# Performance work log

Hardware: AMD Instinct MI355X
Metric: run time of the kernel (lower is better)

The kernel has to match this reference:

```python
import jax, jax.numpy as jnp
import numpy as np

GROUPS = 8
EPS = 1e-5


def group_norm(x, gamma, beta):
    # x: (b, c, h, w); normalize per sample over each group of c//GROUPS channels and all spatial dims
    b, c, h, w = x.shape
    xg = x.reshape(b, GROUPS, c // GROUPS, h, w)
    mean = jnp.mean(xg, axis=(2, 3, 4), keepdims=True)
    var = jnp.var(xg, axis=(2, 3, 4), keepdims=True)
    xn = ((xg - mean) * jax.lax.rsqrt(var + EPS)).reshape(b, c, h, w)
    return xn * gamma[None, :, None, None] + beta[None, :, None, None]


def setup_inputs() -> dict:
    key = jax.random.key(0)
    k1, k2, k3 = jax.random.split(key, 3)
    b, c, h, w = 32, 256, 32, 32
    x = jax.random.normal(k1, (b, c, h, w), dtype=jnp.float32)
    qkv_w = jax.random.normal(k2, (3 * c, c), dtype=jnp.float32) * 0.02
    qkv_b = jnp.zeros((3 * c,), dtype=jnp.float32)
    out_w = jax.random.normal(k3, (c, c), dtype=jnp.float32) * 0.02
    out_b = jnp.zeros((c,), dtype=jnp.float32)
    gn_gamma = jnp.ones((c,), dtype=jnp.float32)
    gn_beta = jnp.zeros((c,), dtype=jnp.float32)
    return {"x": x, "gn_gamma": gn_gamma, "gn_beta": gn_beta,
            "qkv_w": qkv_w, "qkv_b": qkv_b, "out_w": out_w, "out_b": out_b}


def reference(x, gn_gamma, gn_beta, qkv_w, qkv_b, out_w, out_b):
    b, c, h, w = x.shape
    xn = group_norm(x, gn_gamma, gn_beta)
    # 1x1 conv == per-pixel linear: (b,c,h,w) x (3c,c) -> (b,3c,h,w)
    qkv = jnp.einsum('bchw,dc->bdhw', xn, qkv_w) + qkv_b[None, :, None, None]
    q, k, v = jnp.split(qkv, 3, axis=1)
    # (b, c, h, w) -> (b, hw, c)
    def tok(t):
        return t.transpose(0, 2, 3, 1).reshape(b, h * w, c)
    q, k, v = tok(q), tok(k), tok(v)
    scale = 1.0 / jnp.sqrt(jnp.asarray(c, dtype=x.dtype))
    scores = jnp.einsum('bnc,bmc->bnm', q, k) * scale  # (b, hw, hw)
    attn = jax.nn.softmax(scores, axis=-1)
    out = jnp.einsum('bnm,bmc->bnc', attn, v)  # (b, hw, c)
    out = out.reshape(b, h, w, c).transpose(0, 3, 1, 2)  # (b, c, h, w)
    out = jnp.einsum('bchw,dc->bdhw', out, out_w) + out_b[None, :, None, None]
    return out + x
```

## Files before the change

kernel.cpp:

```cpp
#include <hip/hip_runtime.h>
#include <hip/hip_bf16.h>
#include <stdint.h>


typedef __bf16 bf16_t;
typedef __bf16 bf16x4 __attribute__((ext_vector_type(4)));
typedef __bf16 bf16x8 __attribute__((ext_vector_type(8)));
typedef float f32x16 __attribute__((ext_vector_type(16)));
typedef _Float16 f16x4 __attribute__((ext_vector_type(4)));

#define MFMA32(a, b, c) __builtin_amdgcn_mfma_f32_32x32x16_bf16((a), (b), (c), 0, 0, 0)
#define GLL16(g, l)                                                                      \
    __builtin_amdgcn_global_load_lds((const __attribute__((address_space(1))) void*)(g), \
                                     (__attribute__((address_space(3))) void*)(l), 16, 0, 0)
#define WAITV0 asm volatile("s_waitcnt vmcnt(0)" ::: "memory")
#define SBAR   __builtin_amdgcn_s_barrier()

#define QSCALE 0.0901684400555f

__global__ void cast_w(const float* __restrict__ s1, bf16_t* __restrict__ d1, int n1,
                       const float* __restrict__ s2, bf16_t* __restrict__ d2, int n2) {
    int i = blockIdx.x * blockDim.x + threadIdx.x;
    int stride = gridDim.x * blockDim.x;
    for (int k = i; k < n1; k += stride) d1[k] = (bf16_t)s1[k];
    for (int k = i; k < n2; k += stride) d2[k] = (bf16_t)s2[k];
}

__global__ __launch_bounds__(512) void gn_kernel(const float* __restrict__ x,
                                                 const float* __restrict__ gamma,
                                                 const float* __restrict__ beta,
                                                 bf16_t* __restrict__ xn) {
    extern __shared__ char gsm[];
    float* red = (float*)(gsm + 65536);
    int bg = blockIdx.x, b = bg >> 3, g = bg & 7;
    const float* base = x + (size_t)(b * 256 + g * 32) * 1024;
    int tid = threadIdx.x;
    int half = tid >> 8, col = tid & 255;

    float s = 0.f, ss = 0.f;
    #pragma unroll 4
    for (int c2 = 0; c2 < 16; c2++) {
        int c = c2 * 2 + half;
        float4 v = *(const float4*)(base + c * 1024 + col * 4);
        s += v.x + v.y + v.z + v.w;
        ss += v.x * v.x + v.y * v.y + v.z * v.z + v.w * v.w;
        f16x4 h = {(_Float16)v.x, (_Float16)v.y, (_Float16)v.z, (_Float16)v.w};
        *(f16x4*)(gsm + c * 2048 + ((col * 8) ^ ((c & 7) << 4))) = h;
    }
    for (int off = 32; off; off >>= 1) { s += __shfl_down(s, off); ss += __shfl_down(ss, off); }
    if ((tid & 63) == 0) { red[tid >> 6] = s; red[8 + (tid >> 6)] = ss; }
    __syncthreads();
    float S = 0.f, SS = 0.f;
    #pragma unroll
    for (int k = 0; k < 8; k++) { S += red[k]; SS += red[8 + k]; }
    float mean = S * (1.0f / 32768.0f);
    float var = SS * (1.0f / 32768.0f) - mean * mean;
    float rstd = rsqrtf(var + 1e-5f);

    int c = tid & 31;
    float gam = gamma[g * 32 + c] * rstd;
    float bet = beta[g * 32 + c] - mean * gam;
    bf16_t* dst = xn + (size_t)(b * 1024) * 256 + g * 32 + c;
    #pragma unroll 4
    for (int it = 0; it < 64; it++) {
        int p = it * 16 + (tid >> 5);
        _Float16 hv = *(_Float16*)(gsm + c * 2048 + ((p * 2) ^ ((c & 7) << 4)));
        dst[(size_t)p * 256] = (bf16_t)((float)hv * gam + bet);
    }
}

__global__ __launch_bounds__(512, 2) void gemm_qkv(const bf16_t* __restrict__ xn,
                                                   const bf16_t* __restrict__ wq,
                                                   const float* __restrict__ qkv_b,
                                                   bf16_t* __restrict__ qb,
                                                   bf16_t* __restrict__ kb,
                                                   bf16_t* __restrict__ vt) {
    extern __shared__ char smem[];
    char* As = smem;
    int tid = threadIdx.x, wv = tid >> 6, lane = tid & 63;
    int l31 = lane & 31, hi = lane >> 5;
    int t0 = blockIdx.x * 128;
    const char* asrc = (const char*)xn + (size_t)t0 * 512;
    const char* wsrc = (const char*)wq;

    {
        int u = lane & 31, rofs = lane >> 5;
        #pragma unroll
        for (int t = 0; t < 8; t++) {
            int r0 = wv * 16 + t * 2;
            int r = r0 + rofs;
            GLL16(asrc + (size_t)r * 512 + ((u ^ (r & 31)) * 16), As + r0 * 512);
        }
    }
    auto stage_B = [&](int nt) {
        char* Bd = smem + 65536 + (nt & 1) * 32768;
        int u = lane & 31, rofs = lane >> 5;
        #pragma unroll
        for (int t = 0; t < 4; t++) {
            int r0 = wv * 8 + t * 2;
            int r = r0 + rofs;
            GLL16(wsrc + (size_t)(nt * 64 + r) * 512 + ((u ^ (r & 31)) * 16), Bd + r0 * 512);
        }
    };
    stage_B(0);
    WAITV0; SBAR;

    int wm = wv >> 1, wd = wv & 1;
    int bb = t0 >> 10, pos0 = t0 & 1023;

    for (int nt = 0; nt < 12; nt++) {
        if (nt < 11) stage_B(nt + 1);
        const char* Bs = smem + 65536 + (nt & 1) * 32768;
        f32x16 acc = {};
        if (nt < 8) {
            __builtin_amdgcn_s_setprio(1);
            #pragma unroll
            for (int ks = 0; ks < 16; ks++) {
                int col = ks * 32 + hi * 16;
                bf16x8 a = *(const bf16x8*)(As + (wm * 32 + l31) * 512 + (col ^ (l31 << 4)));
                bf16x8 bfr = *(const bf16x8*)(Bs + (wd * 32 + l31) * 512 + (col ^ (l31 << 4)));
                acc = MFMA32(a, bfr, acc);
            }
            __builtin_amdgcn_s_setprio(0);
            int d = nt * 64 + wd * 32 + l31;
            bool isq = nt < 4;
            float bias = qkv_b[d];
            bf16_t* dst = isq ? qb : kb;
            int dd = isq ? d : d - 256;
            float sc = isq ? QSCALE : 1.0f;
            #pragma unroll
            for (int r = 0; r < 16; r++) {
                int tok = t0 + wm * 32 + (r & 3) + 8 * (r >> 2) + 4 * hi;
                dst[(size_t)tok * 256 + dd] = (bf16_t)((acc[r] + bias) * sc);
            }
        } else {
            __builtin_amdgcn_s_setprio(1);
            #pragma unroll
            for (int ks = 0; ks < 16; ks++) {
                int col = ks * 32 + hi * 16;
                bf16x8 a = *(const bf16x8*)(As + (wm * 32 + l31) * 512 + (col ^ (l31 << 4)));
                bf16x8 bfr = *(const bf16x8*)(Bs + (wd * 32 + l31) * 512 + (col ^ (l31 << 4)));
                acc = MFMA32(bfr, a, acc);
            }
            __builtin_amdgcn_s_setprio(0);
            int dbase = (nt - 8) * 64 + wd * 32;
            int pos = pos0 + wm * 32 + l31;
            #pragma unroll
            for (int r = 0; r < 16; r++) {
                int d = dbase + (r & 3) + 8 * (r >> 2) + 4 * hi;
                vt[(size_t)bb * 262144 + (size_t)d * 1024 + pos] =
                    (bf16_t)(acc[r] + qkv_b[512 + d]);
            }
        }
        if (nt < 11) { WAITV0; SBAR; }
    }
}

__global__ __launch_bounds__(256, 1) void attn_kernel(const bf16_t* __restrict__ qb,
                                                      const bf16_t* __restrict__ kb,
                                                      const bf16_t* __restrict__ vt,
                                                      bf16_t* __restrict__ ao) {
    extern __shared__ char smem[];
    int tid = threadIdx.x, i = blockIdx.x;
    int b = (i & 7) + ((i >> 6) << 3);
    int qt = (i >> 3) & 7;
    int wv = tid >> 6, lane = tid & 63, l31 = lane & 31, hi = lane >> 5;

    const char* kbase = (const char*)kb + (size_t)b * 524288;
    const char* vbase = (const char*)vt + (size_t)b * 524288;
    char* Pw = smem + 131072 + wv * 4096;

    int qg = qt * 128 + wv * 32 + l31;
    const char* qsrc = (const char*)qb + (size_t)(b * 1024 + qg) * 512;
    bf16x8 qf[16];
    #pragma unroll
    for (int ks = 0; ks < 16; ks++) qf[ks] = *(const bf16x8*)(qsrc + ks * 32 + hi * 16);

    f32x16 o[8] = {};
    float mrun = -1e30f, lrun = 0.f;

    auto stage = [&](int ch) {
        char* Kd = smem + (ch & 1) * 32768;
        char* Vd = smem + 65536 + (ch & 1) * 32768;
        int j0 = ch * 64;
        #pragma unroll
        for (int t = 0; t < 8; t++) {
            int r0 = wv * 16 + t * 2;
            int r = r0 + (lane >> 5), u = lane & 31;
            GLL16(kbase + (size_t)(j0 + r) * 512 + ((u ^ (r & 31)) * 16), Kd + r0 * 512);
        }
        #pragma unroll
        for (int h = 0; h < 2; h++) {
            #pragma unroll
            for (int p = 0; p < 4; p++) {
                int Ls = (tid << 4) + (p << 12);
                int s = Ls ^ (((Ls >> 9) & 31) << 4);
                GLL16(vbase + (size_t)(s >> 6) * 2048 + j0 * 2 + h * 64 + (s & 63),
                      Vd + h * 16384 + (p << 12) + wv * 1024);
            }
        }
    };

    stage(0);
    __syncthreads();

    for (int ch = 0; ch < 16; ch++) {
        const char* Ks = smem + (ch & 1) * 32768;
        const char* Vs = smem + 65536 + (ch & 1) * 32768;
        if (ch < 15) stage(ch + 1);

        f32x16 sv0 = {}, sv1 = {};
        #pragma unroll
        for (int ks = 0; ks < 16; ks++) {
            int col = ks * 32 + hi * 16;
            bf16x8 k0 = *(const bf16x8*)(Ks + l31 * 512 + (col ^ (l31 << 4)));
            bf16x8 k1 = *(const bf16x8*)(Ks + (32 + l31) * 512 + (col ^ (l31 << 4)));
            sv0 = MFMA32(k0, qf[ks], sv0);
            sv1 = MFMA32(k1, qf[ks], sv1);
        }

        float mc = -1e30f;
        #pragma unroll
        for (int r = 0; r < 16; r++) mc = fmaxf(mc, fmaxf(sv0[r], sv1[r]));
        mc = fmaxf(mc, __shfl_xor(mc, 32));
        float mo = mrun;
        float mn = (mc <= mo + 8.0f) ? mo : mc;
        float rs = 0.f;
        #pragma unroll
        for (int r = 0; r < 16; r++) {
            sv0[r] = exp2f(sv0[r] - mn);
            sv1[r] = exp2f(sv1[r] - mn);
            rs += sv0[r] + sv1[r];
        }
        rs += __shfl_xor(rs, 32);
        float al = exp2f(mo - mn);
        lrun = lrun * al + rs;
        mrun = mn;

        #pragma unroll
        for (int rg = 0; rg < 4; rg++) {
            bf16x4 pa, pb;
            #pragma unroll
            for (int r = 0; r < 4; r++) {
                pa[r] = (bf16_t)sv0[rg * 4 + r];
                pb[r] = (bf16_t)sv1[rg * 4 + r];
            }
            int sw = (l31 & 7) << 4;
            *(bf16x4*)(Pw + l31 * 128 + ((rg * 16 + hi * 8) ^ sw)) = pa;
            *(bf16x4*)(Pw + l31 * 128 + ((64 + rg * 16 + hi * 8) ^ sw)) = pb;
        }
        if (__any(mn != mo)) {
            #pragma unroll
            for (int dt = 0; dt < 8; dt++) o[dt] = o[dt] * al;
        }

        #pragma unroll
        for (int pk = 0; pk < 4; pk++) {
            int pcol = (pk * 32 + hi * 16) ^ ((l31 & 7) << 4);
            bf16x8 pf = *(const bf16x8*)(Pw + l31 * 128 + pcol);
            const char* Vh = Vs + (pk >> 1) * 16384;
            #pragma unroll
            for (int dt = 0; dt < 8; dt++) {
                int d = dt * 32 + l31;
                int a = (d * 64 + (pk & 1) * 32 + hi * 16) ^ (((d >> 3) & 31) << 4);
                bf16x8 vf = *(const bf16x8*)(Vh + a);
                o[dt] = MFMA32(vf, pf, o[dt]);
            }
        }
        __syncthreads();
    }

    float inv = 1.0f / lrun;
    char* aod = (char*)ao + (size_t)(b * 1024 + qg) * 512;
    #pragma unroll
    for (int dt = 0; dt < 8; dt++) {
        #pragma unroll
        for (int rg = 0; rg < 4; rg++) {
            bf16x4 w;
            #pragma unroll
            for (int r = 0; r < 4; r++) w[r] = (bf16_t)(o[dt][rg * 4 + r] * inv);
            *(bf16x4*)(aod + dt * 64 + rg * 16 + hi * 8) = w;
        }
    }
}

__global__ __launch_bounds__(512, 2) void gemm_out(const bf16_t* __restrict__ wo,
                                                   const bf16_t* __restrict__ ao,
                                                   const float* __restrict__ out_b,
                                                   const float* __restrict__ x,
                                                   float* __restrict__ out) {
    extern __shared__ char smem[];
    char* Bs = smem;
    int tid = threadIdx.x, wv = tid >> 6, lane = tid & 63;
    int l31 = lane & 31, hi = lane >> 5;
    int t0 = blockIdx.x * 128;
    const char* bsrc = (const char*)ao + (size_t)t0 * 512;
    const char* wsrc = (const char*)wo;

    {
        int u = lane & 31, rofs = lane >> 5;
        #pragma unroll
        for (int t = 0; t < 8; t++) {
            int r0 = wv * 16 + t * 2;
            int r = r0 + rofs;
            GLL16(bsrc + (size_t)r * 512 + ((u ^ (r & 31)) * 16), Bs + r0 * 512);
        }
    }
    auto stage_W = [&](int ct) {
        char* Wd = smem + 65536 + (ct & 1) * 32768;
        int u = lane & 31, rofs = lane >> 5;
        #pragma unroll
        for (int t = 0; t < 4; t++) {
            int r0 = wv * 8 + t * 2;
            int r = r0 + rofs;
            GLL16(wsrc + (size_t)(ct * 64 + r) * 512 + ((u ^ (r & 31)) * 16), Wd + r0 * 512);
        }
    };
    stage_W(0);
    WAITV0; SBAR;

    int wm = wv >> 1, wc = wv & 1;
    int bb = t0 >> 10, pos0 = t0 & 1023;

    for (int ct = 0; ct < 4; ct++) {
        if (ct < 3) stage_W(ct + 1);
        const char* Ws = smem + 65536 + (ct & 1) * 32768;
        f32x16 acc = {};
        __builtin_amdgcn_s_setprio(1);
        #pragma unroll
        for (int ks = 0; ks < 16; ks++) {
            int col = ks * 32 + hi * 16;
            bf16x8 w = *(const bf16x8*)(Ws + (wc * 32 + l31) * 512 + (col ^ (l31 << 4)));
            bf16x8 bf = *(const bf16x8*)(Bs + (wm * 32 + l31) * 512 + (col ^ (l31 << 4)));
            acc = MFMA32(w, bf, acc);
        }
        __builtin_amdgcn_s_setprio(0);
        int pos = pos0 + wm * 32 + l31;
        #pragma unroll
        for (int r = 0; r < 16; r++) {
            int c = ct * 64 + wc * 32 + (r & 3) + 8 * (r >> 2) + 4 * hi;
            size_t idx = ((size_t)bb * 256 + c) * 1024 + pos;
            out[idx] = acc[r] + out_b[c] + x[idx];
        }
        if (ct < 3) { WAITV0; SBAR; }
    }
}

extern "C" void kernel_launch(void* const* d_in, const int* in_sizes, int n_in,
                              void* d_out, int out_size, void* d_ws, size_t ws_size,
                              hipStream_t stream) {
    (void)in_sizes; (void)n_in; (void)out_size; (void)ws_size;
    const float* x      = (const float*)d_in[0];
    const float* gamma  = (const float*)d_in[1];
    const float* beta   = (const float*)d_in[2];
    const float* qkv_w  = (const float*)d_in[3];
    const float* qkv_b  = (const float*)d_in[4];
    const float* out_w  = (const float*)d_in[5];
    const float* out_b  = (const float*)d_in[6];
    float* out = (float*)d_out;

    char* ws = (char*)d_ws;
    const size_t MB16 = 16777216;
    bf16_t* xn  = (bf16_t*)(ws);
    bf16_t* qb  = (bf16_t*)(ws + 1 * MB16);
    bf16_t* kb  = (bf16_t*)(ws + 2 * MB16);
    bf16_t* vt  = (bf16_t*)(ws + 3 * MB16);
    bf16_t* ao  = (bf16_t*)(ws + 4 * MB16);
    bf16_t* wqb = (bf16_t*)(ws + 5 * MB16);
    bf16_t* wob = (bf16_t*)(ws + 5 * MB16 + 393216);

    cast_w<<<256, 256, 0, stream>>>(qkv_w, wqb, 196608, out_w, wob, 65536);
    gn_kernel<<<256, 512, 65600, stream>>>(x, gamma, beta, xn);
    gemm_qkv<<<256, 512, 131072, stream>>>(xn, wqb, qkv_b, qb, kb, vt);
    attn_kernel<<<256, 256, 147456, stream>>>(qb, kb, vt, ao);
    gemm_out<<<256, 512, 131072, stream>>>(wob, ao, out_b, x, out);
}
```

Before: 125.4 us.

## Rewrite attention with 16x16 MFMA tiles, smaller chunks and two blocks per CU

The attention kernel moves from 32x32x16 MFMA to 16x16x32 MFMA, with 16 query rows per wave, 64 queries per block and 32-key chunks. LDS drops from 147KB to 68KB and launch_bounds allows 2 blocks per CU, with 512 blocks launched instead of 256. The aim is higher occupancy and less per-wave register pressure, so memory latency is better hidden. In exchange each wave does less MFMA work per LDS load, K/V are restaged twice as often, and the K/V LDS swizzles are rewritten.

```diff
diff --git a/kernel.cpp b/kernel.cpp
--- a/kernel.cpp
+++ b/kernel.cpp
@@ -6,10 +6,12 @@
 typedef __bf16 bf16_t;
 typedef __bf16 bf16x4 __attribute__((ext_vector_type(4)));
 typedef __bf16 bf16x8 __attribute__((ext_vector_type(8)));
+typedef float f32x4 __attribute__((ext_vector_type(4)));
 typedef float f32x16 __attribute__((ext_vector_type(16)));
 typedef _Float16 f16x4 __attribute__((ext_vector_type(4)));
 
 #define MFMA32(a, b, c) __builtin_amdgcn_mfma_f32_32x32x16_bf16((a), (b), (c), 0, 0, 0)
+#define MFMA16(a, b, c) __builtin_amdgcn_mfma_f32_16x16x32_bf16((a), (b), (c), 0, 0, 0)
 #define GLL16(g, l)                                                                      \
     __builtin_amdgcn_global_load_lds((const __attribute__((address_space(1))) void*)(g), \
                                      (__attribute__((address_space(3))) void*)(l), 16, 0, 0)
@@ -156,131 +158,122 @@
     }
 }
 
-__global__ __launch_bounds__(256, 1) void attn_kernel(const bf16_t* __restrict__ qb,
+__global__ __launch_bounds__(256, 2) void attn_kernel(const bf16_t* __restrict__ qb,
                                                       const bf16_t* __restrict__ kb,
                                                       const bf16_t* __restrict__ vt,
                                                       bf16_t* __restrict__ ao) {
     extern __shared__ char smem[];
     int tid = threadIdx.x, i = blockIdx.x;
-    int b = (i & 7) + ((i >> 6) << 3);
-    int qt = (i >> 3) & 7;
-    int wv = tid >> 6, lane = tid & 63, l31 = lane & 31, hi = lane >> 5;
+    int b = (i & 7) + ((i >> 7) << 3);
+    int qt = (i >> 3) & 15;
+    int wv = tid >> 6, lane = tid & 63;
+    int q15 = lane & 15, g = lane >> 4;
 
     const char* kbase = (const char*)kb + (size_t)b * 524288;
     const char* vbase = (const char*)vt + (size_t)b * 524288;
-    char* Pw = smem + 131072 + wv * 4096;
-
-    int qg = qt * 128 + wv * 32 + l31;
-    const char* qsrc = (const char*)qb + (size_t)(b * 1024 + qg) * 512;
-    bf16x8 qf[16];
+    char* Pw = smem + 65536 + wv * 1024;
+
+    int qrow = qt * 64 + wv * 16 + q15;
+    const char* qsrc = (const char*)qb + (size_t)(b * 1024 + qrow) * 512;
+    bf16x8 qf[8];
     #pragma unroll
-    for (int ks = 0; ks < 16; ks++) qf[ks] = *(const bf16x8*)(qsrc + ks * 32 + hi * 16);
-
-    f32x16 o[8] = {};
+    for (int f = 0; f < 8; f++) qf[f] = *(const bf16x8*)(qsrc + f * 64 + g * 16);
+
+    f32x4 o16[16] = {};
     float mrun = -1e30f, lrun = 0.f;
 
     auto stage = [&](int ch) {
-        char* Kd = smem + (ch & 1) * 32768;
-        char* Vd = smem + 65536 + (ch & 1) * 32768;
-        int j0 = ch * 64;
-        #pragma unroll
-        for (int t = 0; t < 8; t++) {
-            int r0 = wv * 16 + t * 2;
-            int r = r0 + (lane >> 5), u = lane & 31;
-            GLL16(kbase + (size_t)(j0 + r) * 512 + ((u ^ (r & 31)) * 16), Kd + r0 * 512);
-        }
-        #pragma unroll
-        for (int h = 0; h < 2; h++) {
-            #pragma unroll
-            for (int p = 0; p < 4; p++) {
-                int Ls = (tid << 4) + (p << 12);
-                int s = Ls ^ (((Ls >> 9) & 31) << 4);
-                GLL16(vbase + (size_t)(s >> 6) * 2048 + j0 * 2 + h * 64 + (s & 63),
-                      Vd + h * 16384 + (p << 12) + wv * 1024);
-            }
+        char* Kd = smem + (ch & 1) * 16384;
+        char* Vd = smem + 32768 + (ch & 1) * 16384;
+        int j0 = ch * 32;
+        #pragma unroll
+        for (int p = 0; p < 4; p++) {
+            int Ls = tid * 16 + p * 4096;
+            int r = Ls >> 9, u = (Ls >> 4) & 31;
+            int fk = ((r & 7) << 2) ^ (r >> 3);
+            GLL16(kbase + (size_t)(j0 + r) * 512 + ((u ^ fk) << 4),
+                  Kd + p * 4096 + wv * 1024);
+        }
+        #pragma unroll
+        for (int p = 0; p < 4; p++) {
+            int Ls = tid * 16 + p * 4096;
+            int d = Ls >> 6, u2 = (Ls >> 4) & 3;
+            GLL16(vbase + (size_t)d * 2048 + j0 * 2 + ((u2 ^ ((d >> 3) & 3)) << 4),
+                  Vd + p * 4096 + wv * 1024);
         }
     };
 
     stage(0);
     __syncthreads();
 
-    for (int ch = 0; ch < 16; ch++) {
-        const char* Ks = smem + (ch & 1) * 32768;
-        const char* Vs = smem + 65536 + (ch & 1) * 32768;
-        if (ch < 15) stage(ch + 1);
-
-        f32x16 sv0 = {}, sv1 = {};
-        #pragma unroll
-        for (int ks = 0; ks < 16; ks++) {
-            int col = ks * 32 + hi * 16;
-            bf16x8 k0 = *(const bf16x8*)(Ks + l31 * 512 + (col ^ (l31 << 4)));
-            bf16x8 k1 = *(const bf16x8*)(Ks + (32 + l31) * 512 + (col ^ (l31 << 4)));
-            sv0 = MFMA32(k0, qf[ks], sv0);
-            sv1 = MFMA32(k1, qf[ks], sv1);
-        }
-
-        float mc = -1e30f;
-        #pragma unroll
-        for (int r = 0; r < 16; r++) mc = fmaxf(mc, fmaxf(sv0[r], sv1[r]));
+    int fk0 = ((q15 & 7) << 2) ^ (q15 >> 3);
+    int kr1 = 16 + q15;
+    int fk1 = ((kr1 & 7) << 2) ^ (kr1 >> 3);
+
+    for (int ch = 0; ch < 32; ch++) {
+        const char* Ks = smem + (ch & 1) * 16384;
+        const char* Vs = smem + 32768 + (ch & 1) * 16384;
+        if (ch < 31) stage(ch + 1);
+
+        f32x4 sv0 = {}, sv1 = {};
+        #pragma unroll
+        for (int f = 0; f < 8; f++) {
+            int c = f * 4 + g;
+            bf16x8 k0 = *(const bf16x8*)(Ks + q15 * 512 + ((c ^ fk0) << 4));
+            bf16x8 k1 = *(const bf16x8*)(Ks + kr1 * 512 + ((c ^ fk1) << 4));
+            sv0 = MFMA16(k0, qf[f], sv0);
+            sv1 = MFMA16(k1, qf[f], sv1);
+        }
+
+        float mc = fmaxf(fmaxf(fmaxf(sv0[0], sv0[1]), fmaxf(sv0[2], sv0[3])),
+                         fmaxf(fmaxf(sv1[0], sv1[1]), fmaxf(sv1[2], sv1[3])));
+        mc = fmaxf(mc, __shfl_xor(mc, 16));
         mc = fmaxf(mc, __shfl_xor(mc, 32));
         float mo = mrun;
         float mn = (mc <= mo + 8.0f) ? mo : mc;
         float rs = 0.f;
         #pragma unroll
-        for (int r = 0; r < 16; r++) {
+        for (int r = 0; r < 4; r++) {
             sv0[r] = exp2f(sv0[r] - mn);
             sv1[r] = exp2f(sv1[r] - mn);
             rs += sv0[r] + sv1[r];
         }
+        rs += __shfl_xor(rs, 16);
         rs += __shfl_xor(rs, 32);
         float al = exp2f(mo - mn);
         lrun = lrun * al + rs;
         mrun = mn;
 
-        #pragma unroll
-        for (int rg = 0; rg < 4; rg++) {
-            bf16x4 pa, pb;
-            #pragma unroll
-            for (int r = 0; r < 4; r++) {
-                pa[r] = (bf16_t)sv0[rg * 4 + r];
-                pb[r] = (bf16_t)sv1[rg * 4 + r];
-            }
-            int sw = (l31 & 7) << 4;
-            *(bf16x4*)(Pw + l31 * 128 + ((rg * 16 + hi * 8) ^ sw)) = pa;
-            *(bf16x4*)(Pw + l31 * 128 + ((64 + rg * 16 + hi * 8) ^ sw)) = pb;
-        }
+        bf16x4 pa, pb;
+        #pragma unroll
+        for (int r = 0; r < 4; r++) { pa[r] = (bf16_t)sv0[r]; pb[r] = (bf16_t)sv1[r]; }
+        int blk0 = (g >> 1) ^ (q15 & 3);
+        int blk1 = ((g >> 1) + 2) ^ (q15 & 3);
+        *(bf16x4*)(Pw + q15 * 64 + blk0 * 16 + (g & 1) * 8) = pa;
+        *(bf16x4*)(Pw + q15 * 64 + blk1 * 16 + (g & 1) * 8) = pb;
         if (__any(mn != mo)) {
             #pragma unroll
-            for (int dt = 0; dt < 8; dt++) o[dt] = o[dt] * al;
-        }
-
-        #pragma unroll
-        for (int pk = 0; pk < 4; pk++) {
-            int pcol = (pk * 32 + hi * 16) ^ ((l31 & 7) << 4);
-            bf16x8 pf = *(const bf16x8*)(Pw + l31 * 128 + pcol);
-            const char* Vh = Vs + (pk >> 1) * 16384;
-            #pragma unroll
-            for (int dt = 0; dt < 8; dt++) {
-                int d = dt * 32 + l31;
-                int a = (d * 64 + (pk & 1) * 32 + hi * 16) ^ (((d >> 3) & 31) << 4);
-                bf16x8 vf = *(const bf16x8*)(Vh + a);
-                o[dt] = MFMA32(vf, pf, o[dt]);
-            }
+            for (int dt = 0; dt < 16; dt++) o16[dt] = o16[dt] * al;
+        }
+
+        bf16x8 pf = *(const bf16x8*)(Pw + q15 * 64 + ((g ^ (q15 & 3)) << 4));
+        #pragma unroll
+        for (int dt = 0; dt < 16; dt++) {
+            int d = dt * 16 + q15;
+            bf16x8 vf = *(const bf16x8*)(Vs + d * 64 + ((g ^ ((d >> 3) & 3)) << 4));
+            o16[dt] = MFMA16(vf, pf, o16[dt]);
         }
         __syncthreads();
     }
 
     float inv = 1.0f / lrun;
-    char* aod = (char*)ao + (size_t)(b * 1024 + qg) * 512;
+    char* aod = (char*)ao + (size_t)(b * 1024 + qrow) * 512;
     #pragma unroll
-    for (int dt = 0; dt < 8; dt++) {
-        #pragma unroll
-        for (int rg = 0; rg < 4; rg++) {
-            bf16x4 w;
-            #pragma unroll
-            for (int r = 0; r < 4; r++) w[r] = (bf16_t)(o[dt][rg * 4 + r] * inv);
-            *(bf16x4*)(aod + dt * 64 + rg * 16 + hi * 8) = w;
-        }
+    for (int dt = 0; dt < 16; dt++) {
+        bf16x4 w;
+        #pragma unroll
+        for (int r = 0; r < 4; r++) w[r] = (bf16_t)(o16[dt][r] * inv);
+        *(bf16x4*)(aod + dt * 32 + g * 8) = w;
     }
 }
 
@@ -372,6 +365,6 @@
     cast_w<<<256, 256, 0, stream>>>(qkv_w, wqb, 196608, out_w, wob, 65536);
     gn_kernel<<<256, 512, 65600, stream>>>(x, gamma, beta, xn);
     gemm_qkv<<<256, 512, 131072, stream>>>(xn, wqb, qkv_b, qb, kb, vt);
-    attn_kernel<<<256, 256, 147456, stream>>>(qb, kb, vt, ao);
+    attn_kernel<<<512, 256, 69632, stream>>>(qb, kb, vt, ao);
     gemm_out<<<256, 512, 131072, stream>>>(wob, ao, out_b, x, out);
 }
```

Result: slower. 129.4 us (+3.2%).
